# Kernel tuning notes

Measured on AMD Instinct MI355X. Metric: run time of the kernel, lower is better.

The kernel has to match this reference:

```python
import jax, jax.numpy as jnp
import numpy as np

B, T, V, H, E, MAX_OOV = 128, 200, 50257, 256, 128, 50


def setup_inputs() -> dict:
    key = jax.random.key(0)
    ks = jax.random.split(key, 17)
    s = 0.05  # param scale
    return {
        "decoder_input": jax.random.randint(ks[0], (B, 1), 0, V),
        "encoder_outputs": jax.random.normal(ks[1], (B, T, 2 * H), jnp.float32),
        "encoder_idxs": jax.random.randint(ks[2], (B, T), 0, V),
        "prev_state": jax.random.normal(ks[3], (1, B, H), jnp.float32),
        "selective_read": jax.random.normal(ks[4], (B, 1, 2 * H), jnp.float32) * s,
        "step": 1,
        "emb": jax.random.normal(ks[5], (V, E), jnp.float32) * s,
        "W_ih": jax.random.normal(ks[6], (3 * H, E + 2 * H), jnp.float32) * s,
        "W_hh": jax.random.normal(ks[7], (3 * H, H), jnp.float32) * s,
        "b_ih": jax.random.normal(ks[8], (3 * H,), jnp.float32) * s,
        "b_hh": jax.random.normal(ks[9], (3 * H,), jnp.float32) * s,
        "Wi_w": jax.random.normal(ks[10], (H, 2 * H), jnp.float32) * s,
        "Wi_b": jax.random.normal(ks[11], (H,), jnp.float32) * s,
        "Wg_w": jax.random.normal(ks[12], (V, H), jnp.float32) * s,
        "Wg_b": jax.random.normal(ks[13], (V,), jnp.float32) * s,
        "Wc_w": jax.random.normal(ks[14], (H, 2 * H), jnp.float32) * s,
        "Wc_b": jax.random.normal(ks[15], (H,), jnp.float32) * s,
    }


def _gru_cell(x, h, W_ih, W_hh, b_ih, b_hh):
    # torch GRUCell math, gate order r,z,n
    gi = x @ W_ih.T + b_ih
    gh = h @ W_hh.T + b_hh
    i_r, i_z, i_n = jnp.split(gi, 3, axis=-1)
    h_r, h_z, h_n = jnp.split(gh, 3, axis=-1)
    r = jax.nn.sigmoid(i_r + h_r)
    z = jax.nn.sigmoid(i_z + h_z)
    n = jnp.tanh(i_n + r * h_n)
    return (1.0 - z) * n + z * h


def reference(decoder_input, encoder_outputs, encoder_idxs, prev_state, selective_read,
              step, emb, W_ih, W_hh, b_ih, b_hh, Wi_w, Wi_b, Wg_w, Wg_b, Wc_w, Wc_b):
    dtype = encoder_outputs.dtype
    if step == 0:
        prev_state = (encoder_outputs[:, -1] @ Wi_w.T + Wi_b)[None]      # 1,B,H
        selective_read = jnp.zeros((B, 1, 2 * H), dtype)
    embedded = emb[decoder_input[:, 0]]                                   # B,E
    gru_in = jnp.concatenate([selective_read[:, 0], embedded], axis=-1)   # B,2H+E
    decode_hidden = _gru_cell(gru_in, prev_state[0], W_ih, W_hh, b_ih, b_hh)  # B,H

    score_g = decode_hidden @ Wg_w.T + Wg_b                               # B,V
    enc_proj = jnp.tanh(jnp.einsum('bte,he->bth', encoder_outputs, Wc_w) + Wc_b)  # B,T,H
    score_c = jnp.tanh(jnp.einsum('bth,bh->bt', enc_proj, decode_hidden))         # B,T
    score_c = score_c + jnp.where(encoder_idxs == 0, -10000.0, 0.0).astype(dtype)

    probs = jax.nn.softmax(jnp.concatenate([score_g, score_c], axis=1), axis=1)   # B,V+T
    prob_g, prob_c = probs[:, :V], probs[:, V:]
    prob_g = jnp.concatenate([prob_g, jnp.full((B, MAX_OOV), 1e-4, dtype)], axis=1)  # B,V+oov

    # copy-distribution aggregation: scatter-add prob_c by vocab id (replaces one-hot bmm)
    prob_c_to_g = jnp.zeros((B, V + MAX_OOV), dtype).at[
        jnp.arange(B)[:, None], encoder_idxs].add(prob_c)
    prob_out = (prob_c_to_g + prob_g)[:, None, :]                          # B,1,V+oov

    # selective read for next step
    match = (encoder_idxs == decoder_input).astype(dtype)                  # B,T
    tot = match.sum(axis=1, keepdims=True)
    match = jnp.where(tot > 1, match / tot, match)
    prob_appeared = prob_c * match
    selective_read_new = jnp.einsum('bt,bte->be', prob_appeared, encoder_outputs)[:, None, :]  # B,1,2H
    return prob_out, decode_hidden, selective_read_new
```

## Files before the change

### kernel.cpp

```cpp
#include <hip/hip_runtime.h>

typedef __bf16 bf16;
typedef __bf16 bf16x8 __attribute__((ext_vector_type(8)));
typedef float f32x4 __attribute__((ext_vector_type(4)));

#define B_ 128
#define T_ 200
#define V_ 50257
#define H_ 256
#define E_ 128
#define OOV_ 50
#define VO_ 50307
#define NT_G 3142
#define PSTR 3144

__device__ __forceinline__ float sigmoid_(float x) { return 1.0f / (1.0f + __expf(-x)); }
__device__ __forceinline__ float tanh_(float x) { return 1.0f - 2.0f / (__expf(2.0f * x) + 1.0f); }

__global__ void k_cvt_wc(const float* Wc_w, bf16* WcPack) {
    int f = blockIdx.x * 256 + threadIdx.x;
    int lane = f & 63;
    int g = f >> 6;
    int ks2 = g & 1, nt = (g >> 1) & 15, kc = g >> 5;
    int r = lane & 15, q = lane >> 4;
    int n = nt * 16 + r;
    int k = kc * 64 + ks2 * 32 + q * 8;
    const float* src = Wc_w + n * 512 + k;
    float4 v0 = *(const float4*)src;
    float4 v1 = *(const float4*)(src + 4);
    bf16* d = WcPack + f * 8;
    d[0] = (bf16)v0.x; d[1] = (bf16)v0.y; d[2] = (bf16)v0.z; d[3] = (bf16)v0.w;
    d[4] = (bf16)v1.x; d[5] = (bf16)v1.y; d[6] = (bf16)v1.z; d[7] = (bf16)v1.w;
}

__global__ void k_prep(const int* step_p, const float* enc, const float* prev,
                       const float* selread, const int* dec, const float* emb,
                       const float* Wi_w, const float* Wi_b,
                       float* hT, float* ginT) {
    int b = blockIdx.x, t = threadIdx.x;
    int step = step_p[0];
    float h;
    if (step == 0) {
        float acc = Wi_b[t];
        const float* er = enc + (b * T_ + (T_ - 1)) * 512;
        const float* wr = Wi_w + t * 512;
        for (int k = 0; k < 512; ++k) acc += er[k] * wr[k];
        h = acc;
    } else {
        h = prev[b * H_ + t];
    }
    hT[t * B_ + b] = h;
    for (int k = t; k < 512; k += 256)
        ginT[k * B_ + b] = (step == 0) ? 0.0f : selread[b * 512 + k];
    if (t < E_)
        ginT[(512 + t) * B_ + b] = emb[dec[b] * E_ + t];
}

__global__ void k_gemm_gru(const float* W_ih, const float* b_ih,
                           const float* W_hh, const float* b_hh,
                           const float* ginT, const float* hT,
                           float* giT, float* ghT) {
    int g = blockIdx.x * 256 + threadIdx.x;
    int r = g >> 7, b = g & 127;
    float acc = b_ih[r];
    const float* w = W_ih + r * 640;
#pragma unroll 8
    for (int k = 0; k < 640; ++k) acc += w[k] * ginT[k * B_ + b];
    giT[r * B_ + b] = acc;
    float acc2 = b_hh[r];
    const float* w2 = W_hh + r * 256;
#pragma unroll 8
    for (int k = 0; k < 256; ++k) acc2 += w2[k] * hT[k * B_ + b];
    ghT[r * B_ + b] = acc2;
}

__global__ void k_gru_cell(const float* giT, const float* ghT, const float* hT,
                           float* out_dh, bf16* Apack) {
    int b = blockIdx.x, j = threadIdx.x;
    float ir = giT[j * B_ + b], iz = giT[(256 + j) * B_ + b], in_ = giT[(512 + j) * B_ + b];
    float hr = ghT[j * B_ + b], hz = ghT[(256 + j) * B_ + b], hn = ghT[(512 + j) * B_ + b];
    float hp = hT[j * B_ + b];
    float r = sigmoid_(ir + hr);
    float z = sigmoid_(iz + hz);
    float n = tanh_(in_ + r * hn);
    float h = (1.0f - z) * n + z * hp;
    out_dh[b * H_ + j] = h;
    int mt = b >> 4, rr = b & 15, ks = j >> 5, q = (j >> 3) & 3, jj = j & 7;
    Apack[(((mt * 8 + ks) * 64) + (q * 16 + rr)) * 8 + jj] = (bf16)h;
}

__global__ __launch_bounds__(256) void k_score_g(const bf16* Apack, const float* Wg_w,
                                                 const float* Wg_b, float* out_prob,
                                                 float* pg_part) {
    __shared__ bf16 Bs[64 * 264];
    int tid = threadIdx.x;
    int blk = blockIdx.x;
    int n0 = blk * 64;
#pragma unroll
    for (int j = 0; j < 16; ++j) {
        int f = tid + j * 256;
        int row = f >> 6;
        int c4 = f & 63;
        int n = n0 + row;
        float4 v = (n < V_) ? *(const float4*)(Wg_w + n * 256 + c4 * 4)
                            : float4{0.f, 0.f, 0.f, 0.f};
        bf16* d = Bs + row * 264 + c4 * 4;
        d[0] = (bf16)v.x; d[1] = (bf16)v.y; d[2] = (bf16)v.z; d[3] = (bf16)v.w;
    }
    __syncthreads();
    int w = tid >> 6, lane = tid & 63;
    int r = lane & 15, q = lane >> 4;
    int nt = blk * 4 + w;
    int n = n0 + w * 16 + r;
    bool valid = n < V_;
    f32x4 acc[8];
#pragma unroll
    for (int i = 0; i < 8; ++i) acc[i] = (f32x4){0.f, 0.f, 0.f, 0.f};
#pragma unroll
    for (int ks = 0; ks < 8; ++ks) {
        bf16x8 bfr = *(const bf16x8*)(Bs + (w * 16 + r) * 264 + ks * 32 + q * 8);
#pragma unroll
        for (int mt = 0; mt < 8; ++mt) {
            bf16x8 a = *(const bf16x8*)(Apack + ((mt * 8 + ks) * 64 + lane) * 8);
            acc[mt] = __builtin_amdgcn_mfma_f32_16x16x32_bf16(a, bfr, acc[mt], 0, 0, 0);
        }
    }
    float wgb = valid ? Wg_b[n] : 0.0f;
#pragma unroll
    for (int mt = 0; mt < 8; ++mt) {
#pragma unroll
        for (int rg = 0; rg < 4; ++rg) {
            int row = mt * 16 + q * 4 + rg;
            float e = valid ? __expf(acc[mt][rg] + wgb) : 0.0f;
            if (valid) out_prob[row * VO_ + n] = e;
            float sred = e;
            sred += __shfl_xor(sred, 1);
            sred += __shfl_xor(sred, 2);
            sred += __shfl_xor(sred, 4);
            sred += __shfl_xor(sred, 8);
            if (r == 0) pg_part[row * PSTR + nt] = sred;
        }
    }
}

__global__ __launch_bounds__(256) void k_proj_c(const float* enc, const bf16* WcPack,
                                                const float* Wc_b, const float* dh,
                                                const int* idxs, float* expc) {
    __shared__ bf16 As[64 * 80];
    __shared__ bf16 Bs[16384];
    int tid = threadIdx.x;
    int m0 = blockIdx.x * 64;
    int w = tid >> 6, lane = tid & 63;
    int r = lane & 15, q = lane >> 4;
    f32x4 acc[16];
#pragma unroll
    for (int i = 0; i < 16; ++i) acc[i] = (f32x4){0.f, 0.f, 0.f, 0.f};
    for (int kc = 0; kc < 8; ++kc) {
        __syncthreads();
#pragma unroll
        for (int j = 0; j < 4; ++j) {
            int ff = tid + j * 256;
            int row = ff >> 4;
            int c4 = ff & 15;
            float4 v = *(const float4*)(enc + (m0 + row) * 512 + kc * 64 + c4 * 4);
            bf16* d = As + row * 80 + c4 * 4;
            d[0] = (bf16)v.x; d[1] = (bf16)v.y; d[2] = (bf16)v.z; d[3] = (bf16)v.w;
        }
        {
            const float4* src = (const float4*)(WcPack + kc * 16384);
            float4* dst = (float4*)Bs;
#pragma unroll
            for (int j = 0; j < 8; ++j)
                dst[tid + j * 256] = src[tid + j * 256];
        }
        __syncthreads();
#pragma unroll
        for (int ks2 = 0; ks2 < 2; ++ks2) {
            bf16x8 a = *(const bf16x8*)(As + (w * 16 + r) * 80 + ks2 * 32 + q * 8);
#pragma unroll
            for (int nt = 0; nt < 16; ++nt) {
                bf16x8 bfr = *(const bf16x8*)(Bs + ((nt * 2 + ks2) * 64 + lane) * 8);
                acc[nt] = __builtin_amdgcn_mfma_f32_16x16x32_bf16(a, bfr, acc[nt], 0, 0, 0);
            }
        }
    }
#pragma unroll
    for (int rg = 0; rg < 4; ++rg) {
        int row = m0 + w * 16 + q * 4 + rg;
        int b = row / T_;
        float s = 0.0f;
#pragma unroll
        for (int nt = 0; nt < 16; ++nt) {
            int n = nt * 16 + r;
            float pv = tanh_(acc[nt][rg] + Wc_b[n]);
            s += pv * dh[b * H_ + n];
        }
        s += __shfl_xor(s, 1);
        s += __shfl_xor(s, 2);
        s += __shfl_xor(s, 4);
        s += __shfl_xor(s, 8);
        if (r == 0) {
            int t = row - b * T_;
            float sc = tanh_(s);
            if (idxs[b * T_ + t] == 0) sc -= 10000.0f;
            expc[row] = __expf(sc);
        }
    }
}

__global__ void k_rowsum(const float* pg_part, const float* expc, float* inv) {
    __shared__ float red[256];
    int b = blockIdx.x, t = threadIdx.x;
    float s = 0.0f;
    for (int nt = t; nt < NT_G; nt += 256) s += pg_part[b * PSTR + nt];
    if (t < T_) s += expc[b * T_ + t];
    red[t] = s;
    __syncthreads();
    for (int k = 128; k > 0; k >>= 1) {
        if (t < k) red[t] += red[t + k];
        __syncthreads();
    }
    if (t == 0) inv[b] = 1.0f / red[0];
}

__global__ void k_norm(float* out_prob, const float* inv) {
    int i4 = blockIdx.x * 256 + threadIdx.x;
    if (i4 >= (B_ * VO_ / 4)) return;
    float4 vv = ((const float4*)out_prob)[i4];
    float r[4];
    int base = i4 * 4;
#pragma unroll
    for (int c = 0; c < 4; ++c) {
        int idx = base + c;
        int b = idx / VO_;
        int v = idx - b * VO_;
        float x = (c == 0) ? vv.x : (c == 1) ? vv.y : (c == 2) ? vv.z : vv.w;
        r[c] = (v < V_) ? x * inv[b] : 1e-4f;
    }
    ((float4*)out_prob)[i4] = make_float4(r[0], r[1], r[2], r[3]);
}

__global__ void k_scatter_sel(const float* expc, const float* inv, const int* idxs,
                              const int* dec, const float* enc,
                              float* out_prob, float* out_sel) {
    __shared__ float cf[256];
    __shared__ float red[256];
    int b = blockIdx.x, t = threadIdx.x;
    int d = dec[b];
    float iv = inv[b];
    float pc = 0.0f;
    int m = 0;
    if (t < T_) {
        int ix = idxs[b * T_ + t];
        pc = expc[b * T_ + t] * iv;
        atomicAdd(&out_prob[b * VO_ + ix], pc);
        m = (ix == d) ? 1 : 0;
    }
    cf[t] = m ? pc : 0.0f;
    red[t] = m ? 1.0f : 0.0f;
    __syncthreads();
    for (int s = 128; s > 0; s >>= 1) {
        if (t < s) red[t] += red[t + s];
        __syncthreads();
    }
    float tot = red[0];
    float scale = (tot > 1.0f) ? 1.0f / tot : 1.0f;
    float a0 = 0.0f, a1 = 0.0f;
    for (int tt = 0; tt < T_; ++tt) {
        float c = cf[tt];
        if (c != 0.0f) {
            float w = c * scale;
            a0 += w * enc[(b * T_ + tt) * 512 + t];
            a1 += w * enc[(b * T_ + tt) * 512 + t + 256];
        }
    }
    out_sel[b * 512 + t] = a0;
    out_sel[b * 512 + t + 256] = a1;
}

extern "C" void kernel_launch(void* const* d_in, const int* in_sizes, int n_in,
                              void* d_out, int out_size, void* d_ws, size_t ws_size,
                              hipStream_t stream) {
    const int*   dec     = (const int*)d_in[0];
    const float* enc     = (const float*)d_in[1];
    const int*   idxs    = (const int*)d_in[2];
    const float* prev    = (const float*)d_in[3];
    const float* selread = (const float*)d_in[4];
    const int*   step_p  = (const int*)d_in[5];
    const float* emb     = (const float*)d_in[6];
    const float* W_ih    = (const float*)d_in[7];
    const float* W_hh    = (const float*)d_in[8];
    const float* b_ih    = (const float*)d_in[9];
    const float* b_hh    = (const float*)d_in[10];
    const float* Wi_w    = (const float*)d_in[11];
    const float* Wi_b    = (const float*)d_in[12];
    const float* Wg_w    = (const float*)d_in[13];
    const float* Wg_b    = (const float*)d_in[14];
    const float* Wc_w    = (const float*)d_in[15];
    const float* Wc_b    = (const float*)d_in[16];

    float* ws     = (float*)d_ws;
    float* hT     = ws;
    float* ginT   = ws + 32768;
    float* giT    = ws + 114688;
    float* ghT    = ws + 212992;
    float* inv    = ws + 311296;
    float* expc   = ws + 311552;
    float* pgp    = ws + 337152;
    bf16*  Apack  = (bf16*)(ws + 739584);
    bf16*  WcPack = (bf16*)(ws + 755968);

    float* out      = (float*)d_out;
    float* out_prob = out;
    float* out_dh   = out + 6439296;
    float* out_sel  = out + 6439296 + 32768;

    k_cvt_wc<<<64, 256, 0, stream>>>(Wc_w, WcPack);
    k_prep<<<B_, 256, 0, stream>>>(step_p, enc, prev, selread, dec, emb, Wi_w, Wi_b, hT, ginT);
    k_gemm_gru<<<384, 256, 0, stream>>>(W_ih, b_ih, W_hh, b_hh, ginT, hT, giT, ghT);
    k_gru_cell<<<B_, 256, 0, stream>>>(giT, ghT, hT, out_dh, Apack);
    k_score_g<<<786, 256, 0, stream>>>(Apack, Wg_w, Wg_b, out_prob, pgp);
    k_proj_c<<<400, 256, 0, stream>>>(enc, WcPack, Wc_b, out_dh, idxs, expc);
    k_rowsum<<<B_, 256, 0, stream>>>(pgp, expc, inv);
    k_norm<<<(B_ * VO_ / 4 + 255) / 256, 256, 0, stream>>>(out_prob, inv);
    k_scatter_sel<<<B_, 256, 0, stream>>>(expc, inv, idxs, dec, enc, out_prob, out_sel);
}
```

Measured before the change: 287.5 us.

## Retile score_g and proj_c GEMMs to keep A fragments in registers

The vocab-projection kernel now has each block cover 112 vocab columns. Each wave keeps its two 16-row A tiles of the hidden state in registers and reuses each LDS B fragment across two MFMAs, so fewer blocks are launched and redundant global A loads go away. The copy-projection kernel switches to a 4x4 per-wave MFMA tile. It stages half of K of the encoder rows in LDS and reads prepacked Wc fragments straight from global memory instead of copying them through shared memory, with a cross-wave LDS reduction for the row scores. This trades higher register pressure and larger LDS use per block for less redundant traffic and fewer synchronisations.

```diff
diff --git a/kernel.cpp b/kernel.cpp
--- a/kernel.cpp
+++ b/kernel.cpp
@@ -11,26 +11,27 @@
 #define E_ 128
 #define OOV_ 50
 #define VO_ 50307
-#define NT_G 3142
 #define PSTR 3144
+#define NBG 112
+#define NTB 7
+#define GBG 449
+#define TILES_G 3143
 
 __device__ __forceinline__ float sigmoid_(float x) { return 1.0f / (1.0f + __expf(-x)); }
 __device__ __forceinline__ float tanh_(float x) { return 1.0f - 2.0f / (__expf(2.0f * x) + 1.0f); }
 
 __global__ void k_cvt_wc(const float* Wc_w, bf16* WcPack) {
-    int f = blockIdx.x * 256 + threadIdx.x;
-    int lane = f & 63;
-    int g = f >> 6;
-    int ks2 = g & 1, nt = (g >> 1) & 15, kc = g >> 5;
-    int r = lane & 15, q = lane >> 4;
-    int n = nt * 16 + r;
-    int k = kc * 64 + ks2 * 32 + q * 8;
-    const float* src = Wc_w + n * 512 + k;
-    float4 v0 = *(const float4*)src;
-    float4 v1 = *(const float4*)(src + 4);
-    bf16* d = WcPack + f * 8;
-    d[0] = (bf16)v0.x; d[1] = (bf16)v0.y; d[2] = (bf16)v0.z; d[3] = (bf16)v0.w;
-    d[4] = (bf16)v1.x; d[5] = (bf16)v1.y; d[6] = (bf16)v1.z; d[7] = (bf16)v1.w;
+    int gid = blockIdx.x * 256 + threadIdx.x;
+    int n = gid >> 7;
+    int k4 = gid & 127;
+    int k = k4 * 4;
+    float4 v = *(const float4*)(Wc_w + n * 512 + k);
+    int kstep = k >> 5, kin = k & 31;
+    int q = kin >> 3, j0 = kin & 7;
+    int r = n & 15, nt = n >> 4;
+    int lane = q * 16 + r;
+    bf16* d = WcPack + (((nt * 16 + kstep) * 64) + lane) * 8 + j0;
+    d[0] = (bf16)v.x; d[1] = (bf16)v.y; d[2] = (bf16)v.z; d[3] = (bf16)v.w;
 }
 
 __global__ void k_prep(const int* step_p, const float* enc, const float* prev,
@@ -89,15 +90,15 @@
     Apack[(((mt * 8 + ks) * 64) + (q * 16 + rr)) * 8 + jj] = (bf16)h;
 }
 
-__global__ __launch_bounds__(256) void k_score_g(const bf16* Apack, const float* Wg_w,
-                                                 const float* Wg_b, float* out_prob,
-                                                 float* pg_part) {
-    __shared__ bf16 Bs[64 * 264];
+__global__ __launch_bounds__(256, 2) void k_score_g(const bf16* Apack, const float* Wg_w,
+                                                    const float* Wg_b, float* out_prob,
+                                                    float* pg_part) {
+    __shared__ bf16 Bs[NBG * 264];
     int tid = threadIdx.x;
     int blk = blockIdx.x;
-    int n0 = blk * 64;
-#pragma unroll
-    for (int j = 0; j < 16; ++j) {
+    int n0 = blk * NBG;
+#pragma unroll
+    for (int j = 0; j < 28; ++j) {
         int f = tid + j * 256;
         int row = f >> 6;
         int c4 = f & 63;
@@ -107,38 +108,46 @@
         bf16* d = Bs + row * 264 + c4 * 4;
         d[0] = (bf16)v.x; d[1] = (bf16)v.y; d[2] = (bf16)v.z; d[3] = (bf16)v.w;
     }
-    __syncthreads();
     int w = tid >> 6, lane = tid & 63;
     int r = lane & 15, q = lane >> 4;
-    int nt = blk * 4 + w;
-    int n = n0 + w * 16 + r;
-    bool valid = n < V_;
-    f32x4 acc[8];
-#pragma unroll
-    for (int i = 0; i < 8; ++i) acc[i] = (f32x4){0.f, 0.f, 0.f, 0.f};
+    bf16x8 a[2][8];
+#pragma unroll
+    for (int p = 0; p < 2; ++p)
+#pragma unroll
+        for (int ks = 0; ks < 8; ++ks)
+            a[p][ks] = *(const bf16x8*)(Apack + (((2 * w + p) * 8 + ks) * 64 + lane) * 8);
+    __syncthreads();
+    f32x4 acc[14];
+#pragma unroll
+    for (int i = 0; i < 14; ++i) acc[i] = (f32x4){0.f, 0.f, 0.f, 0.f};
 #pragma unroll
     for (int ks = 0; ks < 8; ++ks) {
-        bf16x8 bfr = *(const bf16x8*)(Bs + (w * 16 + r) * 264 + ks * 32 + q * 8);
-#pragma unroll
-        for (int mt = 0; mt < 8; ++mt) {
-            bf16x8 a = *(const bf16x8*)(Apack + ((mt * 8 + ks) * 64 + lane) * 8);
-            acc[mt] = __builtin_amdgcn_mfma_f32_16x16x32_bf16(a, bfr, acc[mt], 0, 0, 0);
-        }
-    }
-    float wgb = valid ? Wg_b[n] : 0.0f;
-#pragma unroll
-    for (int mt = 0; mt < 8; ++mt) {
-#pragma unroll
-        for (int rg = 0; rg < 4; ++rg) {
-            int row = mt * 16 + q * 4 + rg;
-            float e = valid ? __expf(acc[mt][rg] + wgb) : 0.0f;
-            if (valid) out_prob[row * VO_ + n] = e;
-            float sred = e;
-            sred += __shfl_xor(sred, 1);
-            sred += __shfl_xor(sred, 2);
-            sred += __shfl_xor(sred, 4);
-            sred += __shfl_xor(sred, 8);
-            if (r == 0) pg_part[row * PSTR + nt] = sred;
+#pragma unroll
+        for (int nt = 0; nt < NTB; ++nt) {
+            bf16x8 bfr = *(const bf16x8*)(Bs + (nt * 16 + r) * 264 + ks * 32 + q * 8);
+            acc[nt * 2]     = __builtin_amdgcn_mfma_f32_16x16x32_bf16(a[0][ks], bfr, acc[nt * 2], 0, 0, 0);
+            acc[nt * 2 + 1] = __builtin_amdgcn_mfma_f32_16x16x32_bf16(a[1][ks], bfr, acc[nt * 2 + 1], 0, 0, 0);
+        }
+    }
+#pragma unroll
+    for (int nt = 0; nt < NTB; ++nt) {
+        int n = n0 + nt * 16 + r;
+        bool valid = n < V_;
+        float wgb = valid ? Wg_b[n] : 0.0f;
+#pragma unroll
+        for (int p = 0; p < 2; ++p) {
+#pragma unroll
+            for (int rg = 0; rg < 4; ++rg) {
+                int row = (2 * w + p) * 16 + q * 4 + rg;
+                float e = valid ? __expf(acc[nt * 2 + p][rg] + wgb) : 0.0f;
+                if (valid) out_prob[row * VO_ + n] = e;
+                float sred = e;
+                sred += __shfl_xor(sred, 1);
+                sred += __shfl_xor(sred, 2);
+                sred += __shfl_xor(sred, 4);
+                sred += __shfl_xor(sred, 8);
+                if (r == 0) pg_part[row * PSTR + blk * NTB + nt] = sred;
+            }
         }
     }
 }
@@ -146,8 +155,8 @@
 __global__ __launch_bounds__(256) void k_proj_c(const float* enc, const bf16* WcPack,
                                                 const float* Wc_b, const float* dh,
                                                 const int* idxs, float* expc) {
-    __shared__ bf16 As[64 * 80];
-    __shared__ bf16 Bs[16384];
+    __shared__ bf16 As[64 * 264];
+    __shared__ float sred[64 * 4];
     int tid = threadIdx.x;
     int m0 = blockIdx.x * 64;
     int w = tid >> 6, lane = tid & 63;
@@ -155,56 +164,63 @@
     f32x4 acc[16];
 #pragma unroll
     for (int i = 0; i < 16; ++i) acc[i] = (f32x4){0.f, 0.f, 0.f, 0.f};
-    for (int kc = 0; kc < 8; ++kc) {
+    for (int half = 0; half < 2; ++half) {
         __syncthreads();
 #pragma unroll
-        for (int j = 0; j < 4; ++j) {
-            int ff = tid + j * 256;
-            int row = ff >> 4;
-            int c4 = ff & 15;
-            float4 v = *(const float4*)(enc + (m0 + row) * 512 + kc * 64 + c4 * 4);
-            bf16* d = As + row * 80 + c4 * 4;
+        for (int j = 0; j < 16; ++j) {
+            int f = tid + j * 256;
+            int row = f >> 6;
+            int c4 = f & 63;
+            float4 v = *(const float4*)(enc + (m0 + row) * 512 + half * 256 + c4 * 4);
+            bf16* d = As + row * 264 + c4 * 4;
             d[0] = (bf16)v.x; d[1] = (bf16)v.y; d[2] = (bf16)v.z; d[3] = (bf16)v.w;
         }
-        {
-            const float4* src = (const float4*)(WcPack + kc * 16384);
-            float4* dst = (float4*)Bs;
-#pragma unroll
-            for (int j = 0; j < 8; ++j)
-                dst[tid + j * 256] = src[tid + j * 256];
-        }
         __syncthreads();
 #pragma unroll
-        for (int ks2 = 0; ks2 < 2; ++ks2) {
-            bf16x8 a = *(const bf16x8*)(As + (w * 16 + r) * 80 + ks2 * 32 + q * 8);
-#pragma unroll
-            for (int nt = 0; nt < 16; ++nt) {
-                bf16x8 bfr = *(const bf16x8*)(Bs + ((nt * 2 + ks2) * 64 + lane) * 8);
-                acc[nt] = __builtin_amdgcn_mfma_f32_16x16x32_bf16(a, bfr, acc[nt], 0, 0, 0);
+        for (int ks = 0; ks < 8; ++ks) {
+            int kstep = half * 8 + ks;
+            bf16x8 bfr[4];
+#pragma unroll
+            for (int ntl = 0; ntl < 4; ++ntl)
+                bfr[ntl] = *(const bf16x8*)(WcPack + (((w * 4 + ntl) * 16 + kstep) * 64 + lane) * 8);
+#pragma unroll
+            for (int mt = 0; mt < 4; ++mt) {
+                bf16x8 a = *(const bf16x8*)(As + (mt * 16 + r) * 264 + ks * 32 + q * 8);
+#pragma unroll
+                for (int ntl = 0; ntl < 4; ++ntl)
+                    acc[mt * 4 + ntl] = __builtin_amdgcn_mfma_f32_16x16x32_bf16(a, bfr[ntl], acc[mt * 4 + ntl], 0, 0, 0);
             }
         }
     }
 #pragma unroll
-    for (int rg = 0; rg < 4; ++rg) {
-        int row = m0 + w * 16 + q * 4 + rg;
-        int b = row / T_;
-        float s = 0.0f;
-#pragma unroll
-        for (int nt = 0; nt < 16; ++nt) {
-            int n = nt * 16 + r;
-            float pv = tanh_(acc[nt][rg] + Wc_b[n]);
-            s += pv * dh[b * H_ + n];
-        }
-        s += __shfl_xor(s, 1);
-        s += __shfl_xor(s, 2);
-        s += __shfl_xor(s, 4);
-        s += __shfl_xor(s, 8);
-        if (r == 0) {
-            int t = row - b * T_;
-            float sc = tanh_(s);
-            if (idxs[b * T_ + t] == 0) sc -= 10000.0f;
-            expc[row] = __expf(sc);
-        }
+    for (int mt = 0; mt < 4; ++mt) {
+#pragma unroll
+        for (int rg = 0; rg < 4; ++rg) {
+            int rowl = mt * 16 + q * 4 + rg;
+            int row = m0 + rowl;
+            int b = row / T_;
+            float s = 0.0f;
+#pragma unroll
+            for (int ntl = 0; ntl < 4; ++ntl) {
+                int n = (w * 4 + ntl) * 16 + r;
+                float pv = tanh_(acc[mt * 4 + ntl][rg] + Wc_b[n]);
+                s += pv * dh[b * H_ + n];
+            }
+            s += __shfl_xor(s, 1);
+            s += __shfl_xor(s, 2);
+            s += __shfl_xor(s, 4);
+            s += __shfl_xor(s, 8);
+            if (r == 0) sred[rowl * 4 + w] = s;
+        }
+    }
+    __syncthreads();
+    if (tid < 64) {
+        float s = sred[tid * 4] + sred[tid * 4 + 1] + sred[tid * 4 + 2] + sred[tid * 4 + 3];
+        int row = m0 + tid;
+        int b = row / T_, t = row - b * T_;
+        float sc = tanh_(s);
+        if (idxs[b * T_ + t] == 0) sc -= 10000.0f;
+        expc[row] = __expf(sc);
     }
 }
 
@@ -212,7 +228,7 @@
     __shared__ float red[256];
     int b = blockIdx.x, t = threadIdx.x;
     float s = 0.0f;
-    for (int nt = t; nt < NT_G; nt += 256) s += pg_part[b * PSTR + nt];
+    for (int nt = t; nt < TILES_G; nt += 256) s += pg_part[b * PSTR + nt];
     if (t < T_) s += expc[b * T_ + t];
     red[t] = s;
     __syncthreads();
@@ -315,11 +331,11 @@
     float* out_dh   = out + 6439296;
     float* out_sel  = out + 6439296 + 32768;
 
-    k_cvt_wc<<<64, 256, 0, stream>>>(Wc_w, WcPack);
+    k_cvt_wc<<<128, 256, 0, stream>>>(Wc_w, WcPack);
     k_prep<<<B_, 256, 0, stream>>>(step_p, enc, prev, selread, dec, emb, Wi_w, Wi_b, hT, ginT);
     k_gemm_gru<<<384, 256, 0, stream>>>(W_ih, b_ih, W_hh, b_hh, ginT, hT, giT, ghT);
     k_gru_cell<<<B_, 256, 0, stream>>>(giT, ghT, hT, out_dh, Apack);
-    k_score_g<<<786, 256, 0, stream>>>(Apack, Wg_w, Wg_b, out_prob, pgp);
+    k_score_g<<<GBG, 256, 0, stream>>>(Apack, Wg_w, Wg_b, out_prob, pgp);
     k_proj_c<<<400, 256, 0, stream>>>(enc, WcPack, Wc_b, out_dh, idxs, expc);
     k_rowsum<<<B_, 256, 0, stream>>>(pgp, expc, inv);
     k_norm<<<(B_ * VO_ / 4 + 255) / 256, 256, 0, stream>>>(out_prob, inv);
```

New measurement: 293.8 us. 1.02x slower.
